# Performance work log

Measured on AMD Instinct MI355X. Metric: run time of the kernel, lower is better.

## Reference

```python
import jax, jax.numpy as jnp
import numpy as np

N = 100000   # nodes
E = 600000   # edges (no self loops by construction)
F = 64       # feature_size
H = 2 * F    # hidden_size = 128
G = 32       # graphs in batch
L = N // G   # nodes per graph (equal-size graphs)
NEG_SLOPE = 0.2  # GATConv default leaky_relu slope


def setup_inputs() -> dict:
    key = jax.random.key(0)
    ks = jax.random.split(key, 16)
    x = jax.random.normal(ks[0], (N, F), jnp.float32)
    # edges guaranteed to have no self loops (PyG GAT removes then re-adds them)
    src = jax.random.randint(ks[1], (E,), 0, N)
    off = jax.random.randint(ks[2], (E,), 1, N)
    dst = (src + off) % N
    edge_index = jnp.stack([src, dst]).astype(jnp.int32)
    batch = (jnp.arange(N) // L).astype(jnp.int32)
    sF = 1.0 / np.sqrt(F)
    sH = 1.0 / np.sqrt(H)
    return {
        "x": x, "edge_index": edge_index, "batch": batch,
        "W0": jax.random.normal(ks[3], (F, H), jnp.float32) * sF,
        "b0": jnp.zeros((H,), jnp.float32),
        "Wg": jax.random.normal(ks[4], (H, H), jnp.float32) * sH,
        "att_src": jax.random.normal(ks[5], (H,), jnp.float32) * sH,
        "att_dst": jax.random.normal(ks[6], (H,), jnp.float32) * sH,
        "W1": jax.random.normal(ks[7], (H, H), jnp.float32) * sH,
        "b1": jnp.zeros((H,), jnp.float32),
        "W2": jax.random.normal(ks[8], (H, H), jnp.float32) * sH,
        "b2": jnp.zeros((H,), jnp.float32),
        "Wr": jax.random.normal(ks[9], (H, F), jnp.float32) * sH,
        "br": jnp.zeros((F,), jnp.float32),
    }


def _gcn(x, row, col, w, W, b):
    # PyG GCNConv (normalize=True); edges already include self loops, w holds edge weights.
    xw = x @ W
    deg = jax.ops.segment_sum(w, col, num_segments=N)
    dinv = jnp.where(deg > 0, deg, 1.0) ** -0.5
    dinv = jnp.where(deg > 0, dinv, 0.0)
    norm = dinv[row] * w * dinv[col]                      # [E+N]
    out = jax.ops.segment_sum(xw[row] * norm[:, None], col, num_segments=N)
    return out + b


def reference(x, edge_index, batch, W0, b0, Wg, att_src, att_dst, W1, b1, W2, b2, Wr, br):
    row, col = edge_index[0], edge_index[1]
    loops = jnp.arange(N, dtype=edge_index.dtype)
    row_f = jnp.concatenate([row, loops])                 # [E+N] with self loops
    col_f = jnp.concatenate([col, loops])

    # initial GCNConv (gcn_norm adds self loops with weight 1) + relu
    x = jax.nn.relu(_gcn(x, row_f, col_f, jnp.ones(E + N, x.dtype), W0, b0))

    # GATConv attention (heads=1); node output is discarded in the torch module
    xg = x @ Wg
    a_s = xg @ att_src
    a_d = xg @ att_dst
    e = jax.nn.leaky_relu(a_s[row_f] + a_d[col_f], NEG_SLOPE)
    m = jax.ops.segment_max(e, col_f, num_segments=N)
    ex = jnp.exp(e - m[col_f])
    alpha = ex / jax.ops.segment_sum(ex, col_f, num_segments=N)[col_f]

    # gcn_norm's add_remaining_self_loops replaces self-loop weights with 1.0
    w = alpha.at[E:].set(1.0)

    x = jax.nn.relu(_gcn(x, row_f, col_f, w, W1, b1))
    x = jax.nn.relu(_gcn(x, row_f, col_f, w, W2, b2))

    # readout: Dropout (eval -> identity) + Linear
    out = x @ Wr + br                                     # [N, F]

    # unbatch + pad_sequence (batch_first=True); batch ids are sorted
    counts = jax.ops.segment_sum(jnp.ones(N, jnp.int32), batch, num_segments=G)
    starts = jnp.concatenate([jnp.zeros(1, jnp.int32), jnp.cumsum(counts)[:-1].astype(jnp.int32)])
    pos = jnp.arange(N, dtype=jnp.int32) - starts[batch]
    emb = jnp.zeros((G, L, F), out.dtype).at[batch, pos].set(out)
    return emb
```

## Files before the change

### kernel.cpp

```cpp
#include <hip/hip_runtime.h>
#include <hip/hip_bf16.h>
#include <hip/hip_fp16.h>
#include <math.h>

#define NN 100000
#define EE 600000
#define FF 64
#define HH 128
#define CHUNK 1024
#define NCHUNK ((NN + CHUNK - 1) / CHUNK)
#define NCHUNKS_M (NN / 16)
#define PREP_ITEMS (NN * FF / 4 + 49280)

typedef unsigned short u16;
typedef unsigned int u32;
typedef __attribute__((ext_vector_type(8))) short bf16x8;
typedef __attribute__((ext_vector_type(4))) float f32x4;

__device__ __forceinline__ u16 f2bf(float f) {
    __hip_bfloat16 h = __float2bfloat16(f);
    return *(u16*)&h;
}
__device__ __forceinline__ float bf2f(u16 u) {
    unsigned int t = ((unsigned int)u) << 16;
    return *(float*)&t;
}
__device__ __forceinline__ u32 enc_meta(int r, float w) {
    u16 hb = __half_as_ushort(__float2half(w));
    return ((u32)r << 15) | (hb & 0x7fffu);
}
__device__ __forceinline__ void dec_meta(u32 u, int& r, float& w) {
    r = (int)(u >> 15);
    w = __half2float(__ushort_as_half((u16)(u & 0x7fffu)));
}


__global__ void build_k(const int* __restrict__ col, int* __restrict__ cnt,
                        const float* __restrict__ W0, const float* __restrict__ W1,
                        const float* __restrict__ W2, const float* __restrict__ Wr,
                        const float* __restrict__ Wg, const float* __restrict__ att_src,
                        const float* __restrict__ att_dst, const float* __restrict__ x,
                        u16* __restrict__ Wt0, u16* __restrict__ Wt1,
                        u16* __restrict__ Wt2, u16* __restrict__ Wtr,
                        float* __restrict__ vs, float* __restrict__ vd,
                        u16* __restrict__ xb) {
    int i = blockIdx.x * 256 + threadIdx.x;
    if (i < EE) {
        atomicAdd(&cnt[col[i]], 1);
        return;
    }
    i -= EE;
    if (i < NN * FF / 4) {
        float4 v = ((const float4*)x)[i];
        ushort4 o;
        o.x = f2bf(v.x); o.y = f2bf(v.y); o.z = f2bf(v.z); o.w = f2bf(v.w);
        ((ushort4*)xb)[i] = o;
        return;
    }
    i -= NN * FF / 4;
    if (i < 8192) {
        int n = i >> 6, k = i & 63;
        Wt0[i] = f2bf(W0[k * 128 + n]);
        return;
    }
    i -= 8192;
    if (i < 16384) {
        int n = i >> 7, k = i & 127;
        Wt1[i] = f2bf(W1[k * 128 + n]);
        return;
    }
    i -= 16384;
    if (i < 16384) {
        int n = i >> 7, k = i & 127;
        Wt2[i] = f2bf(W2[k * 128 + n]);
        return;
    }
    i -= 16384;
    if (i < 8192) {
        int n = i >> 7, k = i & 127;
        Wtr[i] = f2bf(Wr[k * 64 + n]);
        return;
    }
    i -= 8192;
    if (i < HH) {
        float s1 = 0.f, s2 = 0.f;
        for (int j = 0; j < HH; j++) {
            float w = Wg[i * HH + j];
            s1 += w * att_src[j];
            s2 += w * att_dst[j];
        }
        vs[i] = s1;
        vd[i] = s2;
    }
}

__global__ void chunksum_k(const int* __restrict__ cnt, int* __restrict__ chunk_sum,
                           float* __restrict__ dinv1) {
    int b = blockIdx.x, t = threadIdx.x;
    int base = b * CHUNK + t * 4;
    int s = 0;
    #pragma unroll
    for (int i = 0; i < 4; i++) {
        int idx = base + i;
        if (idx < NN) {
            int cv = cnt[idx];
            s += cv;
            dinv1[idx] = rsqrtf((float)cv + 1.0f);
        }
    }
    __shared__ int sm[4];
    for (int d = 32; d > 0; d >>= 1) s += __shfl_down(s, d);
    if ((t & 63) == 0) sm[t >> 6] = s;
    __syncthreads();
    if (t == 0) chunk_sum[b] = sm[0] + sm[1] + sm[2] + sm[3];
}

__global__ void chunkoff_k(const int* __restrict__ chunk_sum, int* __restrict__ chunk_off,
                           int* __restrict__ col_ptr) {
    if (threadIdx.x == 0) {
        int run = 0;
        for (int i = 0; i < NCHUNK; i++) { chunk_off[i] = run; run += chunk_sum[i]; }
        col_ptr[NN] = run;
    }
}

__global__ void colptr_k(const int* __restrict__ cnt, const int* __restrict__ chunk_off,
                         int* __restrict__ col_ptr, int* __restrict__ cursor) {
    int b = blockIdx.x, t = threadIdx.x;
    int base = b * CHUNK + t * 4;
    int c[4]; int tot = 0;
    #pragma unroll
    for (int i = 0; i < 4; i++) { int idx = base + i; c[i] = (idx < NN) ? cnt[idx] : 0; tot += c[i]; }
    __shared__ int s[256];
    s[t] = tot;
    __syncthreads();
    for (int d = 1; d < 256; d <<= 1) {
        int v = (t >= d) ? s[t - d] : 0;
        __syncthreads();
        s[t] += v;
        __syncthreads();
    }
    int excl = s[t] - tot;
    int off = chunk_off[b] + excl;
    int pre = 0;
    #pragma unroll
    for (int i = 0; i < 4; i++) {
        int idx = base + i;
        if (idx < NN) {
            col_ptr[idx] = off + pre;
            cursor[idx] = off + pre;
        }
        pre += c[i];
    }
}

__global__ void fill_k(const int* __restrict__ row, const int* __restrict__ col,
                       int* __restrict__ cursor, const float* __restrict__ dinv1,
                       u32* __restrict__ meta1) {
    int e = blockIdx.x * 256 + threadIdx.x;
    if (e < EE) {
        int r = row[e], c = col[e];
        int slot = atomicAdd(&cursor[c], 1);
        meta1[slot] = enc_meta(r, dinv1[r] * dinv1[c]);
    }
}


__global__ __launch_bounds__(256) void aggx_k(
    const u16* __restrict__ xb, const int* __restrict__ col_ptr, const u32* __restrict__ meta1,
    const float* __restrict__ dinv1, u16* __restrict__ xout) {
    int wid = threadIdx.x >> 6, lane = threadIdx.x & 63;
    int sub = lane >> 5;
    int c = blockIdx.x * 8 + wid * 2 + sub;
    int hl = lane & 31;
    int g = hl >> 3;
    int ch = (hl & 7) << 3;
    int beg = col_ptr[c], end = col_ptr[c + 1];
    float acc[8] = {};

    int p = beg + g;
    int r = 0; float w = 0.f;
    if (p < end) dec_meta(meta1[p], r, w);
    while (p < end) {
        bf16x8 v = *(const bf16x8*)&xb[(size_t)r * FF + ch];
        int p2 = p + 4;
        int r2 = 0; float w2 = 0.f;
        if (p2 < end) dec_meta(meta1[p2], r2, w2);
        #pragma unroll
        for (int j = 0; j < 8; j++) acc[j] = fmaf(bf2f((u16)v[j]), w, acc[j]);
        p = p2; r = r2; w = w2;
    }
    #pragma unroll
    for (int j = 0; j < 8; j++) {
        acc[j] += __shfl_xor(acc[j], 8);
        acc[j] += __shfl_xor(acc[j], 16);
    }

    if (g == 0) {
        bf16x8 v = *(const bf16x8*)&xb[(size_t)c * FF + ch];
        float dc = dinv1[c];
        float ws = dc * dc;
        bf16x8 o;
        #pragma unroll
        for (int j = 0; j < 8; j++) {
            float t = fmaf(bf2f((u16)v[j]), ws, acc[j]);
            o[j] = (short)f2bf(t);
        }
        *(bf16x8*)&xout[(size_t)c * FF + ch] = o;
    }
}


__global__ __launch_bounds__(256) void gemm1_k(const u16* __restrict__ A, const u16* __restrict__ Wt,
                                               const float* __restrict__ bias,
                                               const float* __restrict__ vs, const float* __restrict__ vd,
                                               u16* __restrict__ C, float* __restrict__ a_s,
                                               float* __restrict__ a_d) {
    constexpr int K = FF, N = HH, KK = K / 32, NT = N / 16;
    int lane = threadIdx.x & 63;
    int l15 = lane & 15, l4 = lane >> 4;
    int wg = blockIdx.x * 4 + (threadIdx.x >> 6);
    int nwaves = gridDim.x * 4;

    bf16x8 a_frag[KK][NT];
    #pragma unroll
    for (int kk = 0; kk < KK; kk++)
        #pragma unroll
        for (int nt = 0; nt < NT; nt++)
            a_frag[kk][nt] = *(const bf16x8*)&Wt[(size_t)(nt * 16 + l15) * K + kk * 32 + l4 * 8];
    f32x4 bias_f[NT], vs_f[NT], vd_f[NT];
    #pragma unroll
    for (int nt = 0; nt < NT; nt++) {
        bias_f[nt] = *(const f32x4*)&bias[nt * 16 + l4 * 4];
        vs_f[nt] = *(const f32x4*)&vs[nt * 16 + l4 * 4];
        vd_f[nt] = *(const f32x4*)&vd[nt * 16 + l4 * 4];
    }

    for (int ch = wg; ch < NCHUNKS_M; ch += nwaves) {
        int row = ch * 16 + l15;
        bf16x8 b_frag[KK];
        #pragma unroll
        for (int kk = 0; kk < KK; kk++)
            b_frag[kk] = *(const bf16x8*)&A[(size_t)row * K + kk * 32 + l4 * 8];
        f32x4 acc[NT] = {};
        #pragma unroll
        for (int kk = 0; kk < KK; kk++)
            #pragma unroll
            for (int nt = 0; nt < NT; nt++)
                acc[nt] = __builtin_amdgcn_mfma_f32_16x16x32_bf16(a_frag[kk][nt], b_frag[kk],
                                                                  acc[nt], 0, 0, 0);
        float s1 = 0.f, s2 = 0.f;
        #pragma unroll
        for (int nt = 0; nt < NT; nt++) {
            float o0 = fmaxf(acc[nt][0] + bias_f[nt][0], 0.f);
            float o1 = fmaxf(acc[nt][1] + bias_f[nt][1], 0.f);
            float o2 = fmaxf(acc[nt][2] + bias_f[nt][2], 0.f);
            float o3 = fmaxf(acc[nt][3] + bias_f[nt][3], 0.f);
            ushort4 o;
            o.x = f2bf(o0); o.y = f2bf(o1); o.z = f2bf(o2); o.w = f2bf(o3);
            *(ushort4*)&C[(size_t)row * N + nt * 16 + l4 * 4] = o;
            s1 += o0 * vs_f[nt][0] + o1 * vs_f[nt][1] + o2 * vs_f[nt][2] + o3 * vs_f[nt][3];
            s2 += o0 * vd_f[nt][0] + o1 * vd_f[nt][1] + o2 * vd_f[nt][2] + o3 * vd_f[nt][3];
        }
        s1 += __shfl_xor(s1, 16); s1 += __shfl_xor(s1, 32);
        s2 += __shfl_xor(s2, 16); s2 += __shfl_xor(s2, 32);
        if (l4 == 0) {
            a_s[row] = s1;
            a_d[row] = s2;
        }
    }
}


template <int K, int N, bool OUTF32>
__global__ __launch_bounds__(256) void mfma_gemm_k(const u16* __restrict__ A,
                                                   const u16* __restrict__ Wt,
                                                   const float* __restrict__ bias,
                                                   void* __restrict__ C_) {
    constexpr int KK = K / 32;
    constexpr int NT = N / 16;
    int lane = threadIdx.x & 63;
    int l15 = lane & 15, l4 = lane >> 4;
    int wg = blockIdx.x * 4 + (threadIdx.x >> 6);
    int nwaves = gridDim.x * 4;

    bf16x8 a_frag[KK][NT];
    #pragma unroll
    for (int kk = 0; kk < KK; kk++)
        #pragma unroll
        for (int nt = 0; nt < NT; nt++)
            a_frag[kk][nt] = *(const bf16x8*)&Wt[(size_t)(nt * 16 + l15) * K + kk * 32 + l4 * 8];

    f32x4 bias_f[NT];
    if (OUTF32) {
        #pragma unroll
        for (int nt = 0; nt < NT; nt++)
            bias_f[nt] = *(const f32x4*)&bias[nt * 16 + l4 * 4];
    }

    float* Cf = (float*)C_;
    u16* Cb = (u16*)C_;

    for (int ch = wg; ch < NCHUNKS_M; ch += nwaves) {
        int row = ch * 16 + l15;
        bf16x8 b_frag[KK];
        #pragma unroll
        for (int kk = 0; kk < KK; kk++)
            b_frag[kk] = *(const bf16x8*)&A[(size_t)row * K + kk * 32 + l4 * 8];
        f32x4 acc[NT] = {};
        #pragma unroll
        for (int kk = 0; kk < KK; kk++)
            #pragma unroll
            for (int nt = 0; nt < NT; nt++)
                acc[nt] = __builtin_amdgcn_mfma_f32_16x16x32_bf16(a_frag[kk][nt], b_frag[kk],
                                                                  acc[nt], 0, 0, 0);
        #pragma unroll
        for (int nt = 0; nt < NT; nt++) {
            int col = nt * 16 + l4 * 4;
            if (OUTF32) {
                float4 o;
                o.x = acc[nt][0] + bias_f[nt][0];
                o.y = acc[nt][1] + bias_f[nt][1];
                o.z = acc[nt][2] + bias_f[nt][2];
                o.w = acc[nt][3] + bias_f[nt][3];
                *(float4*)&Cf[(size_t)row * N + col] = o;
            } else {
                ushort4 o;
                o.x = f2bf(acc[nt][0]);
                o.y = f2bf(acc[nt][1]);
                o.z = f2bf(acc[nt][2]);
                o.w = f2bf(acc[nt][3]);
                *(ushort4*)&Cb[(size_t)row * N + col] = o;
            }
        }
    }
}


__global__ __launch_bounds__(256) void attn_k(const int* __restrict__ col_ptr,
                                              const u32* __restrict__ meta1,
                                              const float* __restrict__ a_s,
                                              const float* __restrict__ a_d,
                                              float* __restrict__ alpha,
                                              float* __restrict__ dinv2) {
    int lane = threadIdx.x & 63, wid = threadIdx.x >> 6;
    int grp = lane >> 3, idx = lane & 7;
    int c = blockIdx.x * 32 + wid * 8 + grp;
    if (c >= NN) return;
    int beg = col_ptr[c], end = col_ptr[c + 1];
    float ad = a_d[c];
    float es = a_s[c] + ad;
    es = (es > 0.f) ? es : 0.2f * es;
    float m = (idx == 0) ? es : -1e30f;
    float s = (idx == 0) ? 1.f : 0.f;
    for (int p = beg + idx; p < end; p += 8) {
        float e = a_s[meta1[p] >> 15] + ad;
        e = (e > 0.f) ? e : 0.2f * e;
        alpha[p] = e;
        float mn = fmaxf(m, e);
        s = s * expf(m - mn) + expf(e - mn);
        m = mn;
    }
    #pragma unroll
    for (int d = 1; d < 8; d <<= 1) {
        float mo = __shfl_xor(m, d);
        float so = __shfl_xor(s, d);
        float mn = fmaxf(m, mo);
        s = s * expf(m - mn) + so * expf(mo - mn);
        m = mn;
    }
    float inv = 1.f / s;
    float aself = expf(es - m) * inv;
    float d2 = rsqrtf(2.f - aself);
    if (idx == 0) dinv2[c] = d2;
    float sc = inv * d2;
    for (int p = beg + idx; p < end; p += 8)
        alpha[p] = expf(alpha[p] - m) * sc;
}

__global__ void w2_k(const u32* __restrict__ meta1, const float* __restrict__ dinv2,
                     const float* __restrict__ alpha, u32* __restrict__ meta2) {
    int p = blockIdx.x * 256 + threadIdx.x;
    if (p < EE) {
        u32 u = meta1[p];
        int r = (int)(u >> 15);
        float w = alpha[p] * dinv2[r];
        u16 hb = __half_as_ushort(__float2half(w));
        meta2[p] = (u & 0xffff8000u) | (hb & 0x7fffu);
    }
}


__global__ __launch_bounds__(256) void agg2_k(
    const u16* __restrict__ xw, const int* __restrict__ col_ptr, const u32* __restrict__ meta2,
    const float* __restrict__ dinv2, const float* __restrict__ bias, u16* __restrict__ xout) {
    int wid = threadIdx.x >> 6, lane = threadIdx.x & 63;
    int sub = lane >> 5;
    int c = blockIdx.x * 8 + wid * 2 + sub;
    int hl = lane & 31;
    int g = hl >> 4;
    int ch = (hl & 15) << 3;
    int beg = col_ptr[c], end = col_ptr[c + 1];
    float acc[8] = {};

    int pA = beg + g, pB = pA + 2;
    int rA = 0, rB = 0; float wA = 0.f, wB = 0.f;
    if (pA < end) dec_meta(meta2[pA], rA, wA);
    if (pB < end) dec_meta(meta2[pB], rB, wB);
    while (pA < end) {
        bool hb = pB < end;
        bf16x8 vA = *(const bf16x8*)&xw[(size_t)rA * HH + ch];
        bf16x8 vB;
        if (hb) vB = *(const bf16x8*)&xw[(size_t)rB * HH + ch];
        int pA2 = pA + 4, pB2 = pB + 4;
        int rA2 = 0, rB2 = 0; float wA2 = 0.f, wB2 = 0.f;
        if (pA2 < end) dec_meta(meta2[pA2], rA2, wA2);
        if (pB2 < end) dec_meta(meta2[pB2], rB2, wB2);
        #pragma unroll
        for (int j = 0; j < 8; j++) acc[j] = fmaf(bf2f((u16)vA[j]), wA, acc[j]);
        if (hb) {
            #pragma unroll
            for (int j = 0; j < 8; j++) acc[j] = fmaf(bf2f((u16)vB[j]), wB, acc[j]);
        }
        pA = pA2; pB = pB2; rA = rA2; rB = rB2; wA = wA2; wB = wB2;
    }
    #pragma unroll
    for (int j = 0; j < 8; j++) acc[j] += __shfl_xor(acc[j], 16);

    if (g == 0) {
        bf16x8 v = *(const bf16x8*)&xw[(size_t)c * HH + ch];
        float dc = dinv2[c];
        float ws = dc * dc;
        f32x4 b4a = *(const f32x4*)&bias[ch];
        f32x4 b4b = *(const f32x4*)&bias[ch + 4];
        bf16x8 o;
        #pragma unroll
        for (int j = 0; j < 8; j++) {
            float bj = (j < 4) ? b4a[j] : b4b[j - 4];
            float t = fmaxf(fmaf(bf2f((u16)v[j]), ws, acc[j]) + bj, 0.f);
            o[j] = (short)f2bf(t);
        }
        *(bf16x8*)&xout[(size_t)c * HH + ch] = o;
    }
}


extern "C" void kernel_launch(void* const* d_in, const int* in_sizes, int n_in,
                              void* d_out, int out_size, void* d_ws, size_t ws_size,
                              hipStream_t stream) {
    const float* x = (const float*)d_in[0];
    const int* eidx = (const int*)d_in[1];
    const float* W0 = (const float*)d_in[3];
    const float* b0 = (const float*)d_in[4];
    const float* Wg = (const float*)d_in[5];
    const float* att_src = (const float*)d_in[6];
    const float* att_dst = (const float*)d_in[7];
    const float* W1 = (const float*)d_in[8];
    const float* b1 = (const float*)d_in[9];
    const float* W2 = (const float*)d_in[10];
    const float* b2 = (const float*)d_in[11];
    const float* Wr = (const float*)d_in[12];
    const float* br = (const float*)d_in[13];
    float* out = (float*)d_out;

    const int* erow = eidx;
    const int* ecol = eidx + EE;

    char* p = (char*)d_ws;
    auto alloc = [&](size_t bytes) {
        void* r = (void*)p;
        p += (bytes + 255) & ~(size_t)255;
        return r;
    };
    int* col_ptr = (int*)alloc((NN + 1) * sizeof(int));
    u32* meta1 = (u32*)alloc(EE * sizeof(u32));
    u32* meta2 = (u32*)alloc(EE * sizeof(u32));
    int* cnt = (int*)alloc(NN * sizeof(int));
    int* cursor = (int*)alloc(NN * sizeof(int));
    int* chunk_sum = (int*)alloc(128 * sizeof(int));
    int* chunk_off = (int*)alloc(128 * sizeof(int));
    float* alpha = (float*)alloc(EE * sizeof(float));
    float* dinv1 = (float*)alloc(NN * sizeof(float));
    float* dinv2 = (float*)alloc(NN * sizeof(float));
    float* a_s = (float*)alloc(NN * sizeof(float));
    float* a_d = (float*)alloc(NN * sizeof(float));
    float* vs = (float*)alloc(HH * sizeof(float));
    float* vd = (float*)alloc(HH * sizeof(float));
    u16* Wt0 = (u16*)alloc(8192 * sizeof(u16));
    u16* Wt1 = (u16*)alloc(16384 * sizeof(u16));
    u16* Wt2 = (u16*)alloc(16384 * sizeof(u16));
    u16* Wtr = (u16*)alloc(8192 * sizeof(u16));
    u16* xb = (u16*)alloc((size_t)NN * FF * sizeof(u16));
    u16* xaggb = (u16*)alloc((size_t)NN * FF * sizeof(u16));
    u16* bufA = (u16*)alloc((size_t)NN * HH * sizeof(u16));
    u16* bufB = (u16*)alloc((size_t)NN * HH * sizeof(u16));

    hipMemsetAsync(cnt, 0, NN * sizeof(int), stream);

    build_k<<<(EE + PREP_ITEMS + 255) / 256, 256, 0, stream>>>(
        ecol, cnt, W0, W1, W2, Wr, Wg, att_src, att_dst, x,
        Wt0, Wt1, Wt2, Wtr, vs, vd, xb);
    chunksum_k<<<NCHUNK, 256, 0, stream>>>(cnt, chunk_sum, dinv1);
    chunkoff_k<<<1, 64, 0, stream>>>(chunk_sum, chunk_off, col_ptr);
    colptr_k<<<NCHUNK, 256, 0, stream>>>(cnt, chunk_off, col_ptr, cursor);
    fill_k<<<(EE + 255) / 256, 256, 0, stream>>>(erow, ecol, cursor, dinv1, meta1);

    int aggGrid = NN / 8;
    const int GG = 512;

    aggx_k<<<aggGrid, 256, 0, stream>>>(xb, col_ptr, meta1, dinv1, xaggb);
    gemm1_k<<<GG, 256, 0, stream>>>(xaggb, Wt0, b0, vs, vd, bufA, a_s, a_d);
    attn_k<<<(NN + 31) / 32, 256, 0, stream>>>(col_ptr, meta1, a_s, a_d, alpha, dinv2);
    w2_k<<<(EE + 255) / 256, 256, 0, stream>>>(meta1, dinv2, alpha, meta2);
    mfma_gemm_k<HH, HH, false><<<GG, 256, 0, stream>>>(bufA, Wt1, nullptr, bufB);
    agg2_k<<<aggGrid, 256, 0, stream>>>(bufB, col_ptr, meta2, dinv2, b1, bufA);
    mfma_gemm_k<HH, HH, false><<<GG, 256, 0, stream>>>(bufA, Wt2, nullptr, bufB);
    agg2_k<<<aggGrid, 256, 0, stream>>>(bufB, col_ptr, meta2, dinv2, b2, bufA);
    mfma_gemm_k<HH, FF, true><<<GG, 256, 0, stream>>>(bufA, Wtr, br, out);
}
```

Before: 247.8 us.

## Fuse second GCN weight GEMM into first GEMM via per-wave LDS staging

The first dense layer now keeps its ReLU output tile in per-wave shared memory and immediately multiplies it by W1, writing x@W1 directly. This removes the separate 128x128 GEMM launch and the global write and re-read of the intermediate hidden activations. In exchange, W1 fragments are reloaded from global/cache inside the loop and bias and attention vectors are reloaded per chunk, which raises per-chunk instruction and cache traffic and register pressure.

After: 243.3 us. Within noise of the previous version (-1.8%).

```diff
diff --git a/kernel.cpp b/kernel.cpp
--- a/kernel.cpp
+++ b/kernel.cpp
@@ -211,30 +211,28 @@
 }
 
 
-__global__ __launch_bounds__(256) void gemm1_k(const u16* __restrict__ A, const u16* __restrict__ Wt,
+__global__ __launch_bounds__(256) void gemm1_k(const u16* __restrict__ A,
+                                               const u16* __restrict__ Wt0,
+                                               const u16* __restrict__ Wt1,
                                                const float* __restrict__ bias,
                                                const float* __restrict__ vs, const float* __restrict__ vd,
-                                               u16* __restrict__ C, float* __restrict__ a_s,
+                                               u16* __restrict__ Y, float* __restrict__ a_s,
                                                float* __restrict__ a_d) {
-    constexpr int K = FF, N = HH, KK = K / 32, NT = N / 16;
-    int lane = threadIdx.x & 63;
+    constexpr int K = FF, N = HH, KK = K / 32, NT = N / 16, KK2 = HH / 32;
+    constexpr int LSTRIDE = 136;
+    __shared__ u16 lds[4][16 * LSTRIDE];
+    int lane = threadIdx.x & 63, wid = threadIdx.x >> 6;
     int l15 = lane & 15, l4 = lane >> 4;
-    int wg = blockIdx.x * 4 + (threadIdx.x >> 6);
+    int wg = blockIdx.x * 4 + wid;
     int nwaves = gridDim.x * 4;
+    u16* myl = &lds[wid][0];
 
     bf16x8 a_frag[KK][NT];
     #pragma unroll
     for (int kk = 0; kk < KK; kk++)
         #pragma unroll
         for (int nt = 0; nt < NT; nt++)
-            a_frag[kk][nt] = *(const bf16x8*)&Wt[(size_t)(nt * 16 + l15) * K + kk * 32 + l4 * 8];
-    f32x4 bias_f[NT], vs_f[NT], vd_f[NT];
-    #pragma unroll
-    for (int nt = 0; nt < NT; nt++) {
-        bias_f[nt] = *(const f32x4*)&bias[nt * 16 + l4 * 4];
-        vs_f[nt] = *(const f32x4*)&vs[nt * 16 + l4 * 4];
-        vd_f[nt] = *(const f32x4*)&vd[nt * 16 + l4 * 4];
-    }
+            a_frag[kk][nt] = *(const bf16x8*)&Wt0[(size_t)(nt * 16 + l15) * K + kk * 32 + l4 * 8];
 
     for (int ch = wg; ch < NCHUNKS_M; ch += nwaves) {
         int row = ch * 16 + l15;
@@ -252,21 +250,45 @@
         float s1 = 0.f, s2 = 0.f;
         #pragma unroll
         for (int nt = 0; nt < NT; nt++) {
-            float o0 = fmaxf(acc[nt][0] + bias_f[nt][0], 0.f);
-            float o1 = fmaxf(acc[nt][1] + bias_f[nt][1], 0.f);
-            float o2 = fmaxf(acc[nt][2] + bias_f[nt][2], 0.f);
-            float o3 = fmaxf(acc[nt][3] + bias_f[nt][3], 0.f);
+            f32x4 b4 = *(const f32x4*)&bias[nt * 16 + l4 * 4];
+            f32x4 v4 = *(const f32x4*)&vs[nt * 16 + l4 * 4];
+            f32x4 d4 = *(const f32x4*)&vd[nt * 16 + l4 * 4];
+            float o0 = fmaxf(acc[nt][0] + b4[0], 0.f);
+            float o1 = fmaxf(acc[nt][1] + b4[1], 0.f);
+            float o2 = fmaxf(acc[nt][2] + b4[2], 0.f);
+            float o3 = fmaxf(acc[nt][3] + b4[3], 0.f);
             ushort4 o;
             o.x = f2bf(o0); o.y = f2bf(o1); o.z = f2bf(o2); o.w = f2bf(o3);
-            *(ushort4*)&C[(size_t)row * N + nt * 16 + l4 * 4] = o;
-            s1 += o0 * vs_f[nt][0] + o1 * vs_f[nt][1] + o2 * vs_f[nt][2] + o3 * vs_f[nt][3];
-            s2 += o0 * vd_f[nt][0] + o1 * vd_f[nt][1] + o2 * vd_f[nt][2] + o3 * vd_f[nt][3];
+            *(ushort4*)&myl[l15 * LSTRIDE + nt * 16 + l4 * 4] = o;
+            s1 += o0 * v4[0] + o1 * v4[1] + o2 * v4[2] + o3 * v4[3];
+            s2 += o0 * d4[0] + o1 * d4[1] + o2 * d4[2] + o3 * d4[3];
         }
         s1 += __shfl_xor(s1, 16); s1 += __shfl_xor(s1, 32);
         s2 += __shfl_xor(s2, 16); s2 += __shfl_xor(s2, 32);
         if (l4 == 0) {
             a_s[row] = s1;
             a_d[row] = s2;
+        }
+        bf16x8 b2[KK2];
+        #pragma unroll
+        for (int kk2 = 0; kk2 < KK2; kk2++)
+            b2[kk2] = *(const bf16x8*)&myl[l15 * LSTRIDE + kk2 * 32 + l4 * 8];
+        f32x4 acc2[NT] = {};
+        #pragma unroll
+        for (int kk2 = 0; kk2 < KK2; kk2++)
+            #pragma unroll
+            for (int nt = 0; nt < NT; nt++) {
+                bf16x8 w1f = *(const bf16x8*)&Wt1[(size_t)(nt * 16 + l15) * HH + kk2 * 32 + l4 * 8];
+                acc2[nt] = __builtin_amdgcn_mfma_f32_16x16x32_bf16(w1f, b2[kk2], acc2[nt], 0, 0, 0);
+            }
+        #pragma unroll
+        for (int nt = 0; nt < NT; nt++) {
+            ushort4 o;
+            o.x = f2bf(acc2[nt][0]);
+            o.y = f2bf(acc2[nt][1]);
+            o.z = f2bf(acc2[nt][2]);
+            o.w = f2bf(acc2[nt][3]);
+            *(ushort4*)&Y[(size_t)row * HH + nt * 16 + l4 * 4] = o;
         }
     }
 }
@@ -509,10 +531,9 @@
     const int GG = 512;
 
     aggx_k<<<aggGrid, 256, 0, stream>>>(xb, col_ptr, meta1, dinv1, xaggb);
-    gemm1_k<<<GG, 256, 0, stream>>>(xaggb, Wt0, b0, vs, vd, bufA, a_s, a_d);
+    gemm1_k<<<GG, 256, 0, stream>>>(xaggb, Wt0, Wt1, b0, vs, vd, bufB, a_s, a_d);
     attn_k<<<(NN + 31) / 32, 256, 0, stream>>>(col_ptr, meta1, a_s, a_d, alpha, dinv2);
     w2_k<<<(EE + 255) / 256, 256, 0, stream>>>(meta1, dinv2, alpha, meta2);
-    mfma_gemm_k<HH, HH, false><<<GG, 256, 0, stream>>>(bufA, Wt1, nullptr, bufB);
     agg2_k<<<aggGrid, 256, 0, stream>>>(bufB, col_ptr, meta2, dinv2, b1, bufA);
     mfma_gemm_k<HH, HH, false><<<GG, 256, 0, stream>>>(bufA, Wt2, nullptr, bufB);
     agg2_k<<<aggGrid, 256, 0, stream>>>(bufB, col_ptr, meta2, dinv2, b2, bufA);
```
